# Performance work log

Measured on AMD Instinct MI355X. Metric: run time of the kernel, lower is better.

Reference implementation:

```python
import jax, jax.numpy as jnp
import numpy as np

B, T, C = 2, 2048, 1024
H = 16
HS = C // H  # 64
FF = 4 * C


def setup_inputs() -> dict:
    key = jax.random.key(0)
    ks = jax.random.split(key, 8)
    s = 0.02
    x = jax.random.normal(ks[0], (B, T, C), dtype=jnp.float32)
    # per-head projection weights, stacked: y = einsum('btc,hcd->bhtd', x, W)
    Wq = jax.random.normal(ks[1], (H, C, HS), dtype=jnp.float32) * s
    Wk = jax.random.normal(ks[2], (H, C, HS), dtype=jnp.float32) * s
    Wv = jax.random.normal(ks[3], (H, C, HS), dtype=jnp.float32) * s
    # nn.Linear weight layout: [out, in]
    Wproj = jax.random.normal(ks[4], (C, H * HS), dtype=jnp.float32) * s
    W1 = jax.random.normal(ks[5], (FF, C), dtype=jnp.float32) * s
    b1 = jnp.zeros((FF,), dtype=jnp.float32)
    W2 = jax.random.normal(ks[6], (C, FF), dtype=jnp.float32) * s
    return {"x": x, "Wq": Wq, "Wk": Wk, "Wv": Wv, "Wproj": Wproj,
            "W1": W1, "b1": b1, "W2": W2}


def reference(x, Wq, Wk, Wv, Wproj, W1, b1, W2):
    Bb, Tt, Cc = x.shape
    # --- multi-head causal self-attention ---
    q = jnp.einsum('btc,hcd->bhtd', x, Wq)
    k = jnp.einsum('btc,hcd->bhtd', x, Wk)
    v = jnp.einsum('btc,hcd->bhtd', x, Wv)
    scale = HS ** (-0.5)
    scores = jnp.einsum('bhtd,bhsd->bhts', q, k) * scale  # [B,H,T,T]
    causal_mask = jnp.triu(jnp.ones((Tt, Tt), dtype=bool), k=1)
    scores = jnp.where(causal_mask, -jnp.inf, scores)
    wei = jax.nn.softmax(scores, axis=-1)
    attn = jnp.einsum('bhts,bhsd->bhtd', wei, v)  # [B,H,T,HS]
    attn = attn.transpose(0, 2, 1, 3).reshape(Bb, Tt, H * HS)  # concat heads
    sa = attn @ Wproj.T  # [B,T,C]
    x = x + sa
    # --- SiLU MLP ---
    h = jax.nn.silu(x @ W1.T + b1)
    x = x + h @ W2.T
    return x
```

## Files before the change

kernel.cpp:

```cpp
#include <hip/hip_runtime.h>

#define BB 2
#define TT 2048
#define CC 1024
#define HH 16
#define HS 64
#define FF 4096
#define MTOK 4096

typedef __attribute__((ext_vector_type(4))) float f32x4;
typedef __attribute__((ext_vector_type(8))) short short8;

__device__ __forceinline__ unsigned short f2b(float f) {
  unsigned int u = __builtin_bit_cast(unsigned int, f);
  u += 0x7fffu + ((u >> 16) & 1u);
  return (unsigned short)(u >> 16);
}

__device__ __forceinline__ float fast_exp2(float x) {
#if __has_builtin(__builtin_amdgcn_exp2f)
  return __builtin_amdgcn_exp2f(x);
#else
  return exp2f(x);
#endif
}

__device__ __forceinline__ unsigned int cvt_pk_bf16(float lo, float hi) {
  unsigned int r;
  asm("v_cvt_pk_bf16_f32 %0, %1, %2" : "=v"(r) : "v"(lo), "v"(hi));
  return r;
}

__global__ void cast_all_kernel(const float* __restrict__ x,
                                const float* __restrict__ wp,
                                const float* __restrict__ w1,
                                const float* __restrict__ w2,
                                unsigned short* __restrict__ xb,
                                unsigned short* __restrict__ wpb,
                                unsigned short* __restrict__ w1b,
                                unsigned short* __restrict__ w2b) {
  int i = blockIdx.x * 256 + threadIdx.x;
  const float* src;
  unsigned short* dst;
  int off;
  if (i < 524288) {
    src = x; dst = xb; off = i;
  } else if (i < 655360) {
    src = wp; dst = wpb; off = i - 524288;
  } else if (i < 1179648) {
    src = w1; dst = w1b; off = i - 655360;
  } else if (i < 1703936) {
    src = w2; dst = w2b; off = i - 1179648;
  } else {
    return;
  }
  f32x4 a = reinterpret_cast<const f32x4*>(src)[2 * off];
  f32x4 b = reinterpret_cast<const f32x4*>(src)[2 * off + 1];
  short8 o;
  o[0] = (short)f2b(a[0]); o[1] = (short)f2b(a[1]);
  o[2] = (short)f2b(a[2]); o[3] = (short)f2b(a[3]);
  o[4] = (short)f2b(b[0]); o[5] = (short)f2b(b[1]);
  o[6] = (short)f2b(b[2]); o[7] = (short)f2b(b[3]);
  reinterpret_cast<short8*>(dst)[off] = o;
}

__global__ void prep_wqkv_kernel(const float* __restrict__ wq,
                                 const float* __restrict__ wk,
                                 const float* __restrict__ wv,
                                 unsigned short* __restrict__ dst) {
  __shared__ float tile[64][65];
  const int qkv = blockIdx.y >> 4;
  const int h = blockIdx.y & 15;
  const int c0 = blockIdx.x * 64;
  const float* w = (qkv == 0) ? wq : (qkv == 1) ? wk : wv;
  const float scale = (qkv == 0) ? 0.125f : 1.0f;
  const int dd = threadIdx.x & 63;
  const int rr = threadIdx.x >> 6;
  const float* src = w + ((size_t)h * 1024 + c0) * 64;
#pragma unroll
  for (int it = 0; it < 16; ++it) {
    int c = it * 4 + rr;
    tile[c][dd] = src[(size_t)c * 64 + dd];
  }
  __syncthreads();
  unsigned short* dbase = dst + ((size_t)(qkv * 1024 + h * 64)) * 1024 + c0;
#pragma unroll
  for (int it = 0; it < 16; ++it) {
    int d = it * 4 + rr;
    dbase[(size_t)d * 1024 + dd] = f2b(tile[dd][d] * scale);
  }
}

template <int EPI>
__global__ __launch_bounds__(512) void gemm_bt(
    const unsigned short* __restrict__ A, const unsigned short* __restrict__ Bt,
    const int K, const int N, const float* __restrict__ bias,
    const float* __restrict__ resid, float* __restrict__ outf,
    unsigned short* __restrict__ outb, unsigned short* __restrict__ qout,
    unsigned short* __restrict__ kout, unsigned short* __restrict__ vout) {
  __shared__ __align__(16) unsigned short ldsA[3][128 * 64];
  __shared__ __align__(16) unsigned short ldsB[3][128 * 64];
  const int tid = threadIdx.x;
  const int lane = tid & 63;
  const int wave = tid >> 6;
  const int g = lane >> 4, l16 = lane & 15;
  const int wr = wave >> 2;
  const int wc = wave & 3;

  const int gx = gridDim.x;
  const int gy = gridDim.y;
  const int lid = blockIdx.y * gx + blockIdx.x;
  const int xcd = lid & 7;
  const int ii = lid >> 3;
  const int LBM = gy >> 3;
  const int W = LBM * 8;
  const int gwin = ii / W;
  const int jj = ii % W;
  const int bm = xcd * LBM + (jj % LBM);
  const int bn = gwin * 8 + (jj / LBM);

  const int srow = lane >> 3;
  const int schunk = (lane & 7) ^ srow;

  f32x4 acc[4][2] = {};

  const size_t a_row0 = (size_t)bm * 128;
  const size_t b_row0 = (size_t)bn * 128;

  auto STAGE = [&](int step, int buf) {
    const int kt = step * 64;
#pragma unroll
    for (int i = 0; i < 2; ++i) {
      const int row = (wave * 2 + i) * 8 + srow;
      const unsigned short* ga = A + (a_row0 + row) * K + kt + schunk * 8;
      __builtin_amdgcn_global_load_lds(
          (const __attribute__((address_space(1))) unsigned int*)ga,
          (__attribute__((address_space(3))) unsigned int*)(ldsA[buf] + (wave * 2 + i) * 512),
          16, 0, 0);
      const unsigned short* gb = Bt + (b_row0 + row) * K + kt + schunk * 8;
      __builtin_amdgcn_global_load_lds(
          (const __attribute__((address_space(1))) unsigned int*)gb,
          (__attribute__((address_space(3))) unsigned int*)(ldsB[buf] + (wave * 2 + i) * 512),
          16, 0, 0);
    }
  };

  const int nsteps = K >> 6;
  STAGE(0, 0);
  STAGE(1, 1);
  int buf = 0;
  for (int t = 0; t < nsteps; ++t) {
    if (t < nsteps - 1) {
      asm volatile("s_waitcnt vmcnt(4)" ::: "memory");
    } else {
      asm volatile("s_waitcnt vmcnt(0)" ::: "memory");
    }
    __builtin_amdgcn_s_barrier();
    asm volatile("" ::: "memory");
    const unsigned short* bA = ldsA[buf];
    const unsigned short* bB = ldsB[buf];
    short8 af[4][2], bfr[2][2];
#pragma unroll
    for (int mi = 0; mi < 4; ++mi)
#pragma unroll
      for (int ks = 0; ks < 2; ++ks) {
        int row = wr * 64 + mi * 16 + l16;
        int ch = (ks * 4 + g) ^ (row & 7);
        af[mi][ks] = *reinterpret_cast<const short8*>(&bA[row * 64 + ch * 8]);
      }
#pragma unroll
    for (int ni = 0; ni < 2; ++ni)
#pragma unroll
      for (int ks = 0; ks < 2; ++ks) {
        int row = wc * 32 + ni * 16 + l16;
        int ch = (ks * 4 + g) ^ (row & 7);
        bfr[ni][ks] = *reinterpret_cast<const short8*>(&bB[row * 64 + ch * 8]);
      }
    if (t + 2 < nsteps) {
      int nb = buf + 2;
      if (nb >= 3) nb -= 3;
      STAGE(t + 2, nb);
    }
    __builtin_amdgcn_s_setprio(1);
#pragma unroll
    for (int ks = 0; ks < 2; ++ks)
#pragma unroll
      for (int mi = 0; mi < 4; ++mi)
#pragma unroll
        for (int ni = 0; ni < 2; ++ni)
          acc[mi][ni] = __builtin_amdgcn_mfma_f32_16x16x32_bf16(
              af[mi][ks], bfr[ni][ks], acc[mi][ni], 0, 0, 0);
    __builtin_amdgcn_s_setprio(0);
    buf = (buf == 2) ? 0 : buf + 1;
  }

#pragma unroll
  for (int mi = 0; mi < 4; ++mi) {
#pragma unroll
    for (int ni = 0; ni < 2; ++ni) {
#pragma unroll
      for (int j = 0; j < 4; ++j) {
        const int row = bm * 128 + wr * 64 + mi * 16 + g * 4 + j;
        const int col = bn * 128 + wc * 32 + ni * 16 + l16;
        float v = acc[mi][ni][j];
        if (EPI == 0) {
          int qkv = col >> 10;
          int hd = col & 1023;
          int h = hd >> 6, d = hd & 63;
          int b = row >> 11, t = row & 2047;
          size_t base = (size_t)(b * HH + h) * (TT * HS);
          if (qkv == 0) {
            qout[base + ((size_t)t << 6) + d] = f2b(v);
          } else if (qkv == 1) {
            size_t off = ((size_t)((t >> 4) * 2 + (d >> 5)) << 9) +
                         ((((d >> 3) & 3) * 16 + (t & 15)) << 3) + (d & 7);
            kout[base + off] = f2b(v);
          } else {
            size_t off = ((size_t)((t >> 6) * 8 + ((d >> 4) << 1) + ((t & 63) >> 5)) << 9) +
                         ((((t >> 3) & 3) * 16 + (d & 15)) << 3) + (t & 7);
            vout[base + off] = f2b(v);
          }
        } else if (EPI == 1) {
          size_t idx = (size_t)row * N + col;
          float r = resid[idx] + v;
          outf[idx] = r;
          outb[idx] = f2b(r);
        } else if (EPI == 2) {
          float pre = v + bias[col];
          float sg = 1.0f / (1.0f + __expf(-pre));
          outb[(size_t)row * N + col] = f2b(pre * sg);
        } else {
          size_t idx = (size_t)row * N + col;
          outf[idx] += v;
        }
      }
    }
  }
}

#define PSTRIDE 66
__global__ __launch_bounds__(256, 4) void attn_fwd(
    const unsigned short* __restrict__ qg, const unsigned short* __restrict__ kg,
    const unsigned short* __restrict__ vtg, unsigned short* __restrict__ att) {
  __shared__ __align__(16) unsigned short plds[4][16 * PSTRIDE];
  __shared__ float olds[4][16][65];
  __shared__ float mlds[4][16], llds[4][16];
  const int lane = threadIdx.x & 63;
  const int wave = threadIdx.x >> 6;
  const int g = lane >> 4, l16 = lane & 15;
  const int bid = blockIdx.x;
  const int bh = (bid & 7) * 4 + ((bid >> 3) & 3);
  const int b = bh >> 4, h = bh & 15;
  const int pi = wave >> 1, split = wave & 1;
  const int pr = (bid >> 5) * 2 + pi;
  const unsigned short* qh = qg + (size_t)bh * (TT * HS);
  const unsigned short* kh = kg + (size_t)bh * (TT * HS);
  const unsigned short* vth = vtg + (size_t)bh * (TT * HS);
  unsigned short* pw = plds[wave];
  const float L2E = 1.4426950408889634f;

  for (int half = 0; half < 2; ++half) {
    const int tile = half ? (127 - pr) : pr;
    const int r0 = tile * 16;

    short8 qf[2];
#pragma unroll
    for (int ks = 0; ks < 2; ++ks)
      qf[ks] = *reinterpret_cast<const short8*>(
          qh + (size_t)(r0 + l16) * 64 + ks * 32 + g * 8);

    f32x4 oacc[4] = {};
    float mrow = -1e30f, lrow = 0.f;

    const int nkt = (r0 + 79) >> 6;
    for (int kt = split; kt < nkt; kt += 2) {
      const int s0 = kt << 6;
      short8 kf[4][2];
#pragma unroll
      for (int ni = 0; ni < 4; ++ni)
#pragma unroll
        for (int ks = 0; ks < 2; ++ks)
          kf[ni][ks] = *reinterpret_cast<const short8*>(
              kh + (((size_t)(kt * 4 + ni) * 2 + ks) << 9) + lane * 8);
      f32x4 s[4] = {};
      __builtin_amdgcn_s_setprio(1);
#pragma unroll
      for (int ks = 0; ks < 2; ++ks)
#pragma unroll
        for (int ni = 0; ni < 4; ++ni)
          s[ni] = __builtin_amdgcn_mfma_f32_16x16x32_bf16(kf[ni][ks], qf[ks],
                                                          s[ni], 0, 0, 0);
      __builtin_amdgcn_s_setprio(0);
      short8 vf[4][2];
#pragma unroll
      for (int dn = 0; dn < 4; ++dn)
#pragma unroll
        for (int ks = 0; ks < 2; ++ks)
          vf[dn][ks] = *reinterpret_cast<const short8*>(
              vth + (((size_t)(kt * 8 + dn * 2 + ks)) << 9) + lane * 8);
      if (kt == nkt - 1) {
        const int sq = r0 + l16;
#pragma unroll
        for (int ni = 0; ni < 4; ++ni)
#pragma unroll
          for (int j = 0; j < 4; ++j) {
            int sk = s0 + ni * 16 + g * 4 + j;
            if (sk > sq) s[ni][j] = -1e30f;
          }
      }
      float t0 = fmaxf(fmaxf(s[0][0], s[0][1]), fmaxf(s[0][2], s[0][3]));
      float t1 = fmaxf(fmaxf(s[1][0], s[1][1]), fmaxf(s[1][2], s[1][3]));
      float t2 = fmaxf(fmaxf(s[2][0], s[2][1]), fmaxf(s[2][2], s[2][3]));
      float t3 = fmaxf(fmaxf(s[3][0], s[3][1]), fmaxf(s[3][2], s[3][3]));
      float cm = fmaxf(fmaxf(t0, t1), fmaxf(t2, t3));
      cm = fmaxf(cm, __shfl_xor(cm, 16));
      cm = fmaxf(cm, __shfl_xor(cm, 32));
      if (__any(cm > mrow + 8.0f)) {
        float mnew = fmaxf(mrow, cm);
        float sc = fast_exp2((mrow - mnew) * L2E);
        mrow = mnew;
        lrow *= sc;
#pragma unroll
        for (int j = 0; j < 4; ++j) {
          float scj = __shfl(sc, g * 4 + j);
#pragma unroll
          for (int dn = 0; dn < 4; ++dn) oacc[dn][j] *= scj;
        }
      }
      const float mL = mrow * L2E;
#pragma unroll
      for (int ni = 0; ni < 4; ++ni)
#pragma unroll
        for (int j = 0; j < 4; ++j)
          s[ni][j] = fast_exp2(__builtin_fmaf(s[ni][j], L2E, -mL));
      float a0 = (s[0][0] + s[0][1]) + (s[0][2] + s[0][3]);
      float a1 = (s[1][0] + s[1][1]) + (s[1][2] + s[1][3]);
      float a2 = (s[2][0] + s[2][1]) + (s[2][2] + s[2][3]);
      float a3 = (s[3][0] + s[3][1]) + (s[3][2] + s[3][3]);
      float ps = (a0 + a1) + (a2 + a3);
      ps += __shfl_xor(ps, 16);
      ps += __shfl_xor(ps, 32);
      lrow += ps;
#pragma unroll
      for (int ni = 0; ni < 4; ++ni) {
        unsigned int w0 = cvt_pk_bf16(s[ni][0], s[ni][1]);
        unsigned int w1 = cvt_pk_bf16(s[ni][2], s[ni][3]);
        unsigned int* pd =
            reinterpret_cast<unsigned int*>(&pw[l16 * PSTRIDE + ni * 16 + g * 4]);
        pd[0] = w0;
        pd[1] = w1;
      }
      asm volatile("" ::: "memory");
      short8 pa[2];
#pragma unroll
      for (int ks = 0; ks < 2; ++ks)
        pa[ks] = *reinterpret_cast<const short8*>(&pw[l16 * PSTRIDE + ks * 32 + g * 8]);
      __builtin_amdgcn_s_setprio(1);
#pragma unroll
      for (int ks = 0; ks < 2; ++ks)
#pragma unroll
        for (int dn = 0; dn < 4; ++dn)
          oacc[dn] = __builtin_amdgcn_mfma_f32_16x16x32_bf16(pa[ks], vf[dn][ks],
                                                             oacc[dn], 0, 0, 0);
      __builtin_amdgcn_s_setprio(0);
      asm volatile("" ::: "memory");
    }
#pragma unroll
    for (int dn = 0; dn < 4; ++dn)
#pragma unroll
      for (int j = 0; j < 4; ++j)
        olds[wave][g * 4 + j][dn * 16 + l16] = oacc[dn][j];
    if (lane < 16) {
      mlds[wave][lane] = mrow;
      llds[wave][lane] = lrow;
    }
    __syncthreads();
    if (split == 0) {
#pragma unroll
      for (int j = 0; j < 4; ++j) {
        const int q = g * 4 + j;
        float mA = mlds[wave][q], lA = llds[wave][q];
        float mB = mlds[wave ^ 1][q], lB = llds[wave ^ 1][q];
        float ms = fmaxf(mA, mB);
        float a = fast_exp2((mA - ms) * L2E);
        float bb = fast_exp2((mB - ms) * L2E);
        float rinv = 1.0f / (lA * a + lB * bb);
        int t = r0 + q;
#pragma unroll
        for (int dn = 0; dn < 4; ++dn) {
          float ob = olds[wave ^ 1][q][dn * 16 + l16];
          float val = (oacc[dn][j] * a + ob * bb) * rinv;
          att[((size_t)(b * TT + t)) * CC + h * 64 + dn * 16 + l16] = f2b(val);
        }
      }
    }
    __syncthreads();
  }
}

extern "C" void kernel_launch(void* const* d_in, const int* in_sizes, int n_in,
                              void* d_out, int out_size, void* d_ws, size_t ws_size,
                              hipStream_t stream) {
  const float* x = (const float*)d_in[0];
  const float* Wq = (const float*)d_in[1];
  const float* Wk = (const float*)d_in[2];
  const float* Wv = (const float*)d_in[3];
  const float* Wproj = (const float*)d_in[4];
  const float* W1 = (const float*)d_in[5];
  const float* b1 = (const float*)d_in[6];
  const float* W2 = (const float*)d_in[7];
  float* out = (float*)d_out;
  char* ws = (char*)d_ws;
  const size_t MB = 1024 * 1024;
  unsigned short* xb = (unsigned short*)(ws + 0 * MB);
  unsigned short* wqkvT = (unsigned short*)(ws + 8 * MB);
  unsigned short* wprojb = (unsigned short*)(ws + 14 * MB);
  unsigned short* w1b = (unsigned short*)(ws + 16 * MB);
  unsigned short* w2b = (unsigned short*)(ws + 24 * MB);
  unsigned short* qb = (unsigned short*)(ws + 32 * MB);
  unsigned short* kpk = (unsigned short*)(ws + 40 * MB);
  unsigned short* vpk = (unsigned short*)(ws + 48 * MB);
  unsigned short* att = (unsigned short*)(ws + 64 * MB);
  unsigned short* x1b = (unsigned short*)(ws + 72 * MB);
  unsigned short* hb = (unsigned short*)(ws + 80 * MB);

  cast_all_kernel<<<6656, 256, 0, stream>>>(x, Wproj, W1, W2, xb, wprojb, w1b, w2b);
  prep_wqkv_kernel<<<dim3(16, 48), 256, 0, stream>>>(Wq, Wk, Wv, wqkvT);

  gemm_bt<0><<<dim3(24, 32), 512, 0, stream>>>(xb, wqkvT, 1024, 3072, nullptr,
                                               nullptr, nullptr, nullptr, qb, kpk, vpk);
  attn_fwd<<<1024, 256, 0, stream>>>(qb, kpk, vpk, att);
  gemm_bt<1><<<dim3(8, 32), 512, 0, stream>>>(att, wprojb, 1024, 1024, nullptr,
                                              x, out, x1b, nullptr, nullptr, nullptr);
  gemm_bt<2><<<dim3(32, 32), 512, 0, stream>>>(x1b, w1b, 1024, 4096, b1, nullptr,
                                               nullptr, hb, nullptr, nullptr, nullptr);
  gemm_bt<3><<<dim3(8, 32), 512, 0, stream>>>(hb, w2b, 4096, 1024, nullptr, nullptr,
                                              out, nullptr, nullptr, nullptr, nullptr);
  (void)in_sizes; (void)n_in; (void)out_size; (void)ws_size;
}
```

Before: 205.9 us.

## Add 256x256-tile GEMM kernel for QKV and MLP-up projections

Introduces a gemm256 kernel that computes 256x256 output tiles per 512-thread block, with 8 waves each holding 8x4 MFMA accumulators. It stages K=32 slices via global_load_lds into double-buffered, XOR-swizzled LDS. The QKV and W1 GEMMs switch to it, which quarters the block count and doubles operand reuse per LDS load. The epilogue is factored into a shared helper. The cost is much higher register pressure (128 accumulator floats per lane) and fewer blocks: 192 for QKV and 256 for W1, which may underfill 256 CUs or cause wave-quantization imbalance.

```diff
diff --git a/kernel.cpp b/kernel.cpp
--- a/kernel.cpp
+++ b/kernel.cpp
@@ -92,6 +92,44 @@
 }
 
 template <int EPI>
+__device__ __forceinline__ void gemm_epi(int row, int col, int N, float v,
+                                         const float* bias, const float* resid,
+                                         float* outf, unsigned short* outb,
+                                         unsigned short* qout, unsigned short* kout,
+                                         unsigned short* vout) {
+  if (EPI == 0) {
+    int qkv = col >> 10;
+    int hd = col & 1023;
+    int h = hd >> 6, d = hd & 63;
+    int b = row >> 11, t = row & 2047;
+    size_t base = (size_t)(b * HH + h) * (TT * HS);
+    if (qkv == 0) {
+      qout[base + ((size_t)t << 6) + d] = f2b(v);
+    } else if (qkv == 1) {
+      size_t off = ((size_t)((t >> 4) * 2 + (d >> 5)) << 9) +
+                   ((((d >> 3) & 3) * 16 + (t & 15)) << 3) + (d & 7);
+      kout[base + off] = f2b(v);
+    } else {
+      size_t off = ((size_t)((t >> 6) * 8 + ((d >> 4) << 1) + ((t & 63) >> 5)) << 9) +
+                   ((((t >> 3) & 3) * 16 + (d & 15)) << 3) + (t & 7);
+      vout[base + off] = f2b(v);
+    }
+  } else if (EPI == 1) {
+    size_t idx = (size_t)row * N + col;
+    float r = resid[idx] + v;
+    outf[idx] = r;
+    outb[idx] = f2b(r);
+  } else if (EPI == 2) {
+    float pre = v + bias[col];
+    float sg = 1.0f / (1.0f + __expf(-pre));
+    outb[(size_t)row * N + col] = f2b(pre * sg);
+  } else {
+    size_t idx = (size_t)row * N + col;
+    outf[idx] += v;
+  }
+}
+
+template <int EPI>
 __global__ __launch_bounds__(512) void gemm_bt(
     const unsigned short* __restrict__ A, const unsigned short* __restrict__ Bt,
     const int K, const int N, const float* __restrict__ bias,
@@ -195,47 +233,118 @@
   }
 
 #pragma unroll
-  for (int mi = 0; mi < 4; ++mi) {
-#pragma unroll
-    for (int ni = 0; ni < 2; ++ni) {
+  for (int mi = 0; mi < 4; ++mi)
+#pragma unroll
+    for (int ni = 0; ni < 2; ++ni)
 #pragma unroll
       for (int j = 0; j < 4; ++j) {
         const int row = bm * 128 + wr * 64 + mi * 16 + g * 4 + j;
         const int col = bn * 128 + wc * 32 + ni * 16 + l16;
-        float v = acc[mi][ni][j];
-        if (EPI == 0) {
-          int qkv = col >> 10;
-          int hd = col & 1023;
-          int h = hd >> 6, d = hd & 63;
-          int b = row >> 11, t = row & 2047;
-          size_t base = (size_t)(b * HH + h) * (TT * HS);
-          if (qkv == 0) {
-            qout[base + ((size_t)t << 6) + d] = f2b(v);
-          } else if (qkv == 1) {
-            size_t off = ((size_t)((t >> 4) * 2 + (d >> 5)) << 9) +
-                         ((((d >> 3) & 3) * 16 + (t & 15)) << 3) + (d & 7);
-            kout[base + off] = f2b(v);
-          } else {
-            size_t off = ((size_t)((t >> 6) * 8 + ((d >> 4) << 1) + ((t & 63) >> 5)) << 9) +
-                         ((((t >> 3) & 3) * 16 + (d & 15)) << 3) + (t & 7);
-            vout[base + off] = f2b(v);
-          }
-        } else if (EPI == 1) {
-          size_t idx = (size_t)row * N + col;
-          float r = resid[idx] + v;
-          outf[idx] = r;
-          outb[idx] = f2b(r);
-        } else if (EPI == 2) {
-          float pre = v + bias[col];
-          float sg = 1.0f / (1.0f + __expf(-pre));
-          outb[(size_t)row * N + col] = f2b(pre * sg);
-        } else {
-          size_t idx = (size_t)row * N + col;
-          outf[idx] += v;
-        }
-      }
-    }
-  }
+        gemm_epi<EPI>(row, col, N, acc[mi][ni][j], bias, resid, outf, outb,
+                      qout, kout, vout);
+      }
+}
+
+template <int EPI>
+__global__ __launch_bounds__(512, 2) void gemm256(
+    const unsigned short* __restrict__ A, const unsigned short* __restrict__ Bt,
+    const int K, const int N, const float* __restrict__ bias,
+    const float* __restrict__ resid, float* __restrict__ outf,
+    unsigned short* __restrict__ outb, unsigned short* __restrict__ qout,
+    unsigned short* __restrict__ kout, unsigned short* __restrict__ vout) {
+  __shared__ __align__(16) unsigned short bufA[2][256 * 32];
+  __shared__ __align__(16) unsigned short bufB[2][256 * 32];
+  const int tid = threadIdx.x;
+  const int lane = tid & 63;
+  const int wave = tid >> 6;
+  const int g = lane >> 4, l16 = lane & 15;
+  const int wr = wave >> 2;
+  const int wc = wave & 3;
+
+  const int gx = gridDim.x;
+  const int gy = gridDim.y;
+  const int lid = blockIdx.y * gx + blockIdx.x;
+  const int xcd = lid & 7;
+  const int ii = lid >> 3;
+  const int LBM = gy >> 3;
+  const int W = LBM * 4;
+  const int gwin = ii / W;
+  const int jj = ii % W;
+  const int bm = xcd * LBM + (jj % LBM);
+  const int bn = gwin * 4 + (jj / LBM);
+
+  const int srow = lane >> 2;
+  const int schunk = (lane & 3) ^ (srow & 3);
+
+  f32x4 acc[8][4] = {};
+
+  const size_t a_row0 = (size_t)bm * 256;
+  const size_t b_row0 = (size_t)bn * 256;
+
+  auto STAGE_ALL = [&](int step, int bsel) {
+    const int kt = step * 32;
+#pragma unroll
+    for (int i = 0; i < 2; ++i) {
+      const int row = wave * 32 + i * 16 + srow;
+      const unsigned short* ga = A + (a_row0 + row) * K + kt + schunk * 8;
+      __builtin_amdgcn_global_load_lds(
+          (const __attribute__((address_space(1))) unsigned int*)ga,
+          (__attribute__((address_space(3))) unsigned int*)(bufA[bsel] + (wave * 2 + i) * 512),
+          16, 0, 0);
+      const unsigned short* gb = Bt + (b_row0 + row) * K + kt + schunk * 8;
+      __builtin_amdgcn_global_load_lds(
+          (const __attribute__((address_space(1))) unsigned int*)gb,
+          (__attribute__((address_space(3))) unsigned int*)(bufB[bsel] + (wave * 2 + i) * 512),
+          16, 0, 0);
+    }
+  };
+
+  const int nsteps = K >> 5;
+  STAGE_ALL(0, 0);
+  for (int t = 0; t < nsteps; ++t) {
+    const int cur = t & 1;
+    __syncthreads();
+    if (t + 1 < nsteps) STAGE_ALL(t + 1, cur ^ 1);
+    const unsigned short* bA = bufA[cur];
+    const unsigned short* bB = bufB[cur];
+    short8 bfr[4];
+#pragma unroll
+    for (int ni = 0; ni < 4; ++ni) {
+      int row = wc * 64 + ni * 16 + l16;
+      int ch = g ^ (row & 3);
+      bfr[ni] = *reinterpret_cast<const short8*>(&bB[row * 32 + ch * 8]);
+    }
+#pragma unroll
+    for (int p = 0; p < 4; ++p) {
+      short8 af[2];
+#pragma unroll
+      for (int q = 0; q < 2; ++q) {
+        int row = wr * 128 + (p * 2 + q) * 16 + l16;
+        int ch = g ^ (row & 3);
+        af[q] = *reinterpret_cast<const short8*>(&bA[row * 32 + ch * 8]);
+      }
+      __builtin_amdgcn_s_setprio(1);
+#pragma unroll
+      for (int q = 0; q < 2; ++q)
+#pragma unroll
+        for (int ni = 0; ni < 4; ++ni)
+          acc[p * 2 + q][ni] = __builtin_amdgcn_mfma_f32_16x16x32_bf16(
+              af[q], bfr[ni], acc[p * 2 + q][ni], 0, 0, 0);
+      __builtin_amdgcn_s_setprio(0);
+    }
+  }
+
+#pragma unroll
+  for (int mi = 0; mi < 8; ++mi)
+#pragma unroll
+    for (int ni = 0; ni < 4; ++ni)
+#pragma unroll
+      for (int j = 0; j < 4; ++j) {
+        const int row = bm * 256 + wr * 128 + mi * 16 + g * 4 + j;
+        const int col = bn * 256 + wc * 64 + ni * 16 + l16;
+        gemm_epi<EPI>(row, col, N, acc[mi][ni][j], bias, resid, outf, outb,
+                      qout, kout, vout);
+      }
 }
 
 #define PSTRIDE 66
@@ -427,12 +536,12 @@
   cast_all_kernel<<<6656, 256, 0, stream>>>(x, Wproj, W1, W2, xb, wprojb, w1b, w2b);
   prep_wqkv_kernel<<<dim3(16, 48), 256, 0, stream>>>(Wq, Wk, Wv, wqkvT);
 
-  gemm_bt<0><<<dim3(24, 32), 512, 0, stream>>>(xb, wqkvT, 1024, 3072, nullptr,
+  gemm256<0><<<dim3(12, 16), 512, 0, stream>>>(xb, wqkvT, 1024, 3072, nullptr,
                                                nullptr, nullptr, nullptr, qb, kpk, vpk);
   attn_fwd<<<1024, 256, 0, stream>>>(qb, kpk, vpk, att);
   gemm_bt<1><<<dim3(8, 32), 512, 0, stream>>>(att, wprojb, 1024, 1024, nullptr,
                                               x, out, x1b, nullptr, nullptr, nullptr);
-  gemm_bt<2><<<dim3(32, 32), 512, 0, stream>>>(x1b, w1b, 1024, 4096, b1, nullptr,
+  gemm256<2><<<dim3(16, 16), 512, 0, stream>>>(x1b, w1b, 1024, 4096, b1, nullptr,
                                                nullptr, hb, nullptr, nullptr, nullptr);
   gemm_bt<3><<<dim3(8, 32), 512, 0, stream>>>(hb, w2b, 4096, 1024, nullptr, nullptr,
                                               out, nullptr, nullptr, nullptr, nullptr);
```

Measured after the change: 226.9 us. +10.2%, slower.
